# Optimization experiments

Measured on AMD Instinct MI355X. Metric: run time of the kernel, lower is better.

The kernel has to match this reference:

```python
import jax, jax.numpy as jnp
import numpy as np

BN, S, D = 200, 128, 1024          # B*N entity rows, scenes, d_model
D_INNER, D_STATE, D_CONV = 2048, 32, 4


def setup_inputs() -> dict:
    key = jax.random.key(0)
    ks = jax.random.split(key, 8)
    s = 0.02
    return {
        "x": jax.random.normal(ks[0], (BN, S, D), jnp.float32),
        "emotion_bias": jax.random.uniform(ks[1], (BN, S, 1), jnp.float32),
        "norm_w": jnp.ones((D,), jnp.float32),
        "norm_b": jnp.zeros((D,), jnp.float32),
        "in_proj_W": jax.random.normal(ks[2], (2 * D_INNER, D), jnp.float32) * s,
        "conv_w": jax.random.normal(ks[3], (D_INNER, 1, D_CONV), jnp.float32) * 0.1,
        "conv_b": jnp.zeros((D_INNER,), jnp.float32),
        "x_proj_W": jax.random.normal(ks[4], (2 * D_STATE + 1, D_INNER), jnp.float32) * s,
        "dt_W": jax.random.normal(ks[5], (D_INNER, 1), jnp.float32),
        "dt_b": jnp.zeros((D_INNER,), jnp.float32),
        "out_W": jax.random.normal(ks[6], (D, D_INNER), jnp.float32) * s,
        "emotion_scale": jnp.array(0.1, jnp.float32),
    }


def reference(x, emotion_bias, norm_w, norm_b, in_proj_W, conv_w, conv_b,
              x_proj_W, dt_W, dt_b, out_W, emotion_scale):
    residual = x
    # LayerNorm (eps=1e-5, biased variance as in torch)
    mu = x.mean(-1, keepdims=True)
    var = ((x - mu) ** 2).mean(-1, keepdims=True)
    xn = (x - mu) * jax.lax.rsqrt(var + 1e-5) * norm_w + norm_b

    xz = xn @ in_proj_W.T                      # [BN, S, 2*d_inner]
    x_in, z = jnp.split(xz, 2, axis=-1)

    # causal depthwise conv1d (torch pads d_conv-1 both sides, truncates to S == left-pad only)
    xc = jax.lax.conv_general_dilated(
        x_in.transpose(0, 2, 1), conv_w,
        window_strides=(1,), padding=[(D_CONV - 1, 0)],
        feature_group_count=D_INNER,
        dimension_numbers=("NCH", "OIH", "NCH"))
    xc = (xc + conv_b[None, :, None]).transpose(0, 2, 1)   # [BN, S, d_inner]
    x_act = jax.nn.silu(xc)

    x_ssm = x_act @ x_proj_W.T                 # [BN, S, 2*d_state+1]
    delta_raw, B_mat, C = jnp.split(x_ssm, [1, 1 + D_STATE], axis=-1)
    delta = jax.nn.softplus(delta_raw @ dt_W.T + dt_b)     # [BN, S, d_inner]
    delta = jnp.maximum(delta + emotion_scale * emotion_bias, 1e-4)

    def step(h, inp):
        d_t, B_t, C_t, xa_t = inp              # [BN,d_inner],[BN,n],[BN,n],[BN,d_inner]
        h = h * jnp.exp(-d_t)[..., None] + B_t[:, None, :] * xa_t[..., None]
        h = jnp.clip(h, -100.0, 100.0)
        y_t = jnp.einsum("bdn,bn->bd", h, C_t)
        return h, y_t

    h0 = jnp.zeros((BN, D_INNER, D_STATE), jnp.float32)
    xs = (delta.transpose(1, 0, 2), B_mat.transpose(1, 0, 2),
          C.transpose(1, 0, 2), x_act.transpose(1, 0, 2))
    _, y = jax.lax.scan(step, h0, xs)          # y: [S, BN, d_inner]
    y = y.transpose(1, 0, 2)

    return (y * jax.nn.silu(z)) @ out_W.T + residual
```

## Files before the change

kernel.cpp:

```cpp
#include <hip/hip_runtime.h>
#include <cstdint>
#include <cstddef>

#define NBN   200
#define NS    128
#define ND    1024
#define NDI   2048
#define NST   32
#define NROWS (NBN * NS)

typedef __attribute__((ext_vector_type(8))) short bf16x8;
typedef __attribute__((ext_vector_type(4))) float f32x4;

__device__ __forceinline__ unsigned short f2bf(float f) {
    unsigned int u = __float_as_uint(f);
    u += 0x7fffu + ((u >> 16) & 1u);
    return (unsigned short)(u >> 16);
}
__device__ __forceinline__ float bf2f(unsigned short h) {
    return __uint_as_float(((unsigned int)h) << 16);
}

__device__ __forceinline__ void gl_lds16(const void* g, void* l) {
    typedef __attribute__((address_space(1))) const unsigned int* gp_t;
    typedef __attribute__((address_space(3))) unsigned int* lp_t;
    __builtin_amdgcn_global_load_lds((gp_t)(uintptr_t)g,
                                     (lp_t)(unsigned int)(uintptr_t)l, 16, 0, 0);
}

__global__ __launch_bounds__(256) void cvt_kernel(const float* __restrict__ src,
                                                  unsigned short* __restrict__ dst, int n) {
    int i = blockIdx.x * 256 + threadIdx.x;
    if (i < n) dst[i] = f2bf(src[i]);
}

__global__ __launch_bounds__(256) void padwx_kernel(const float* __restrict__ src,
                                                    unsigned short* __restrict__ dst) {
    int i = blockIdx.x * 256 + threadIdx.x;
    int r = i >> 11;
    dst[i] = (r < 65) ? f2bf(src[i]) : (unsigned short)0;
}

__global__ __launch_bounds__(256) void ln_kernel(const float* __restrict__ x,
                                                 const float* __restrict__ gw,
                                                 const float* __restrict__ gb,
                                                 unsigned short* __restrict__ xn) {
    __shared__ float ss[4], ss2[4];
    size_t row = blockIdx.x;
    int tid = threadIdx.x;
    const float4* px = (const float4*)(x + row * ND);
    float4 v = px[tid];
    float s  = v.x + v.y + v.z + v.w;
    float s2 = fmaf(v.x, v.x, fmaf(v.y, v.y, fmaf(v.z, v.z, v.w * v.w)));
    #pragma unroll
    for (int off = 32; off > 0; off >>= 1) {
        s  += __shfl_down(s,  off, 64);
        s2 += __shfl_down(s2, off, 64);
    }
    if ((tid & 63) == 0) { ss[tid >> 6] = s; ss2[tid >> 6] = s2; }
    __syncthreads();
    float tot  = ss[0] + ss[1] + ss[2] + ss[3];
    float tot2 = ss2[0] + ss2[1] + ss2[2] + ss2[3];
    float mu   = tot * (1.f / ND);
    float var  = fmaf(tot2, 1.f / ND, -mu * mu);
    float rstd = rsqrtf(var + 1e-5f);
    float4 wv = ((const float4*)gw)[tid];
    float4 bv = ((const float4*)gb)[tid];
    ushort4 o;
    o.x = f2bf(fmaf((v.x - mu) * rstd, wv.x, bv.x));
    o.y = f2bf(fmaf((v.y - mu) * rstd, wv.y, bv.y));
    o.z = f2bf(fmaf((v.z - mu) * rstd, wv.z, bv.z));
    o.w = f2bf(fmaf((v.w - mu) * rstd, wv.w, bv.w));
    ((ushort4*)(xn + row * ND))[tid] = o;
}


#define BARRIER __builtin_amdgcn_s_barrier()
#define LGKM0  asm volatile("s_waitcnt lgkmcnt(0)" ::: "memory")
#define VMCNT6 asm volatile("s_waitcnt vmcnt(6)" ::: "memory")
#define VMCNT0 asm volatile("s_waitcnt vmcnt(0)" ::: "memory")
#define NOWAIT ((void)0)
#define PRIO1  __builtin_amdgcn_s_setprio(1)
#define PRIO0  __builtin_amdgcn_s_setprio(0)

#define STG_A(t, kp) {                                                        \
    gl_lds16(gA0 + (size_t)(t) * 64 + (kp) * 32,                              \
             lA + (((t) & 1) << 15) + ((kp) << 14));                          \
    gl_lds16(gA1 + (size_t)(t) * 64 + (kp) * 32,                              \
             lA + (((t) & 1) << 15) + ((kp) << 14) + 8192); }
#define STG_B(t, kp) {                                                        \
    gl_lds16(gB0 + (size_t)(t) * 64 + (kp) * 32,                              \
             lB + (((t) & 1) << 15) + ((kp) << 14));                          \
    gl_lds16(gB1 + (size_t)(t) * 64 + (kp) * 32,                              \
             lB + (((t) & 1) << 15) + ((kp) << 14) + 8192); }

#define RD_A(dst, mh, kp) { _Pragma("unroll")                                 \
    for (int mi = 0; mi < 4; ++mi)                                            \
        dst[mi] = *(const bf16x8*)(aRd + bo + (kp) * 16384 + (mh) * 4096 + mi * 1024); }
#define RD_B(dst, kp) { _Pragma("unroll")                                     \
    for (int ni = 0; ni < 4; ++ni)                                            \
        dst[ni] = *(const bf16x8*)(bRd + bo + (kp) * 16384 + ni * 1024); }

#define MM(mh, AV, BV) { _Pragma("unroll")                                    \
    for (int mi = 0; mi < 4; ++mi) { _Pragma("unroll")                        \
        for (int ni = 0; ni < 4; ++ni)                                        \
            acc[(mh) * 4 + mi][ni] = __builtin_amdgcn_mfma_f32_16x16x32_bf16( \
                AV[mi], BV[ni], acc[(mh) * 4 + mi][ni], 0, 0, 0); } }

#define TILE(t, DO_AP1, DO_T2, W) {                                           \
    const int bo = ((t) & 1) << 15;                                           \
                                                          \
    RD_A(aK0, 0, 0); RD_B(bK0, 0);                                            \
    if (DO_AP1) STG_A((t) + 1, 1);                                            \
    BARRIER; LGKM0; PRIO1; MM(0, aK0, bK0); PRIO0; BARRIER;                   \
                                                          \
    RD_A(aK1, 0, 1); RD_B(bK1, 1);                                            \
    if (DO_T2) STG_B((t) + 2, 0);                                             \
    BARRIER; LGKM0; PRIO1; MM(0, aK1, bK1); PRIO0; BARRIER;                   \
                                                          \
    RD_A(aK0, 1, 0);                                                          \
    if (DO_T2) STG_B((t) + 2, 1);                                             \
    BARRIER; LGKM0; PRIO1; MM(1, aK0, bK0); PRIO0; BARRIER;                   \
                                                          \
    RD_A(aK1, 1, 1);                                                          \
    if (DO_T2) STG_A((t) + 2, 0);                                             \
    BARRIER; LGKM0; PRIO1; MM(1, aK1, bK1); PRIO0;                            \
    W;                                                                        \
    BARRIER; }

template <int K, int EPI>
__global__ __launch_bounds__(512, 2)
void gemm256(const unsigned short* __restrict__ A,
             const unsigned short* __restrict__ B,
             int N, void* __restrict__ outp, const float* __restrict__ resid) {
    constexpr int NT = K / 64;
    static_assert(NT >= 3, "need >=3 K-tiles");
    __shared__ __align__(16) char smem[131072];

    const int tid  = threadIdx.x;
    const int lane = tid & 63;
    const int wid  = tid >> 6;
    const int lrow = lane & 15;
    const int kq   = lane >> 4;
    const int wmi  = wid >> 2;
    const int wni  = wid & 3;

    const int gx  = gridDim.x;
    const int nwg = gx * gridDim.y;
    const int lin = blockIdx.y * gx + blockIdx.x;
    const int id2 = (lin & 7) * (nwg >> 3) + (lin >> 3);
    const int bm  = id2 % gx;
    const int bn  = id2 / gx;

    const size_t m0 = (size_t)bm * 256;
    const size_t n0 = (size_t)bn * 256;

    const int fr = (lrow >> 1) & 3;
    const char* aRd = smem +          (wmi * 128 + lrow) * 64 + ((kq ^ fr) << 4);
    const char* bRd = smem + 65536 + (wni * 64  + lrow) * 64 + ((kq ^ fr) << 4);

    const int srow = wid * 16 + (lane >> 2);
    const int scol = (((lane & 3) ^ ((lane >> 3) & 3)) << 3);
    const unsigned short* gA0 = A + (m0 + srow) * K + scol;
    const unsigned short* gA1 = A + (m0 + 128 + srow) * K + scol;
    const unsigned short* gB0 = B + (n0 + srow) * K + scol;
    const unsigned short* gB1 = B + (n0 + 128 + srow) * K + scol;
    char* lA = smem + wid * 1024;
    char* lB = smem + 65536 + wid * 1024;

    f32x4 acc[8][4];
    #pragma unroll
    for (int i = 0; i < 8; ++i)
        #pragma unroll
        for (int j = 0; j < 4; ++j) acc[i][j] = (f32x4){0.f, 0.f, 0.f, 0.f};

    bf16x8 aK0[4], aK1[4], bK0[4], bK1[4];

    STG_B(0, 0); STG_B(0, 1); STG_A(0, 0); STG_A(0, 1);
    STG_B(1, 0); STG_B(1, 1); STG_A(1, 0);
    VMCNT6;
    BARRIER;

    int t = 0;
    #pragma unroll 2
    for (; t < NT - 2; ++t) { TILE(t, 1, 1, VMCNT6); }
    TILE((NT - 2), 1, 0, VMCNT0);
    TILE((NT - 1), 0, 0, NOWAIT);

    #pragma unroll
    for (int mi = 0; mi < 8; ++mi)
        #pragma unroll
        for (int ni = 0; ni < 4; ++ni)
            #pragma unroll
            for (int r = 0; r < 4; ++r) {
                size_t row = m0 + wmi * 128 + mi * 16 + kq * 4 + r;
                size_t col = n0 + wni * 64 + ni * 16 + lrow;
                size_t idx = row * (size_t)N + col;
                float v = acc[mi][ni][r];
                if (EPI == 0) ((unsigned short*)outp)[idx] = f2bf(v);
                else          ((float*)outp)[idx] = v + resid[idx];
            }
}

__global__ __launch_bounds__(256) void conv_silu_kernel(const unsigned short* __restrict__ xz,
                                                        const float* __restrict__ cw,
                                                        const float* __restrict__ cb,
                                                        unsigned short* __restrict__ xact) {
    int tid = blockIdx.x * 256 + threadIdx.x;
    int c = tid & (NDI - 1);
    int b = tid >> 11;
    float4 wv = ((const float4*)cw)[c];
    float w0 = wv.x, w1 = wv.y, w2 = wv.z, w3 = wv.w;
    float bias = cb[c];
    const unsigned short* px = xz + (size_t)b * NS * (2 * NDI) + c;
    unsigned short* po = xact + (size_t)b * NS * NDI + c;
    float x0 = 0.f, x1 = 0.f, x2 = 0.f;
    for (int t = 0; t < NS; t++) {
        float x3 = bf2f(px[(size_t)t * (2 * NDI)]);
        float v  = fmaf(x3, w3, fmaf(x2, w2, fmaf(x1, w1, fmaf(x0, w0, bias))));
        float s  = v * __builtin_amdgcn_rcpf(1.f + __expf(-v));
        po[(size_t)t * NDI] = f2bf(s);
        x0 = x1; x1 = x2; x2 = x3;
    }
}

__global__ __launch_bounds__(256, 2)
void gemm2_kernel(const unsigned short* __restrict__ A,
                  const unsigned short* __restrict__ B,
                  float* __restrict__ out) {
    __shared__ __align__(16) unsigned short As[64 * 32];
    __shared__ __align__(16) unsigned short Bs[80 * 32];
    const int tid  = threadIdx.x;
    const int bm   = blockIdx.x;
    const int wid  = tid >> 6;
    const int lane = tid & 63;
    const int lrow = lane & 15;
    const int kq   = lane >> 4;

    f32x4 acc[5];
    #pragma unroll
    for (int i = 0; i < 5; i++) acc[i] = (f32x4){0.f, 0.f, 0.f, 0.f};

    const int r1 = tid >> 2;
    const int c8 = (tid & 3) << 3;
    const unsigned short* gA1 = A + ((size_t)bm * 64 + r1) * NDI + c8;
    const unsigned short* gB1 = B + (size_t)r1 * NDI + c8;
    const unsigned short* gB2 = B + (size_t)(64 + r1) * NDI + c8;
    char* lA1 = (char*)As + wid * 1024;
    char* lB1 = (char*)Bs + wid * 1024;
    char* lB2 = (char*)Bs + 4096;

    for (int kt = 0; kt < NDI; kt += 32) {
        __syncthreads();
        gl_lds16(gA1, lA1);
        gl_lds16(gB1, lB1);
        if (tid < 64) gl_lds16(gB2, lB2);
        gA1 += 32; gB1 += 32; gB2 += 32;
        __syncthreads();
        bf16x8 af = *(const bf16x8*)&As[(wid * 16 + lrow) * 32 + kq * 8];
        #pragma unroll
        for (int ni = 0; ni < 5; ni++) {
            bf16x8 bfr = *(const bf16x8*)&Bs[(ni * 16 + lrow) * 32 + kq * 8];
            acc[ni] = __builtin_amdgcn_mfma_f32_16x16x32_bf16(af, bfr, acc[ni], 0, 0, 0);
        }
    }
    #pragma unroll
    for (int ni = 0; ni < 5; ni++)
        #pragma unroll
        for (int r = 0; r < 4; r++) {
            size_t row = (size_t)bm * 64 + wid * 16 + kq * 4 + r;
            int col = ni * 16 + lrow;
            out[row * 80 + col] = acc[ni][r];
        }
}

__global__ __launch_bounds__(256)
void scan_kernel(const float* __restrict__ xssm,
                 unsigned short* xact_g,
                 const unsigned short* __restrict__ xz,
                 const float* __restrict__ dtW,
                 const float* __restrict__ dtb,
                 const float* __restrict__ eb,
                 const float* __restrict__ es_p) {
    __shared__ __align__(16) float sB[NS][NST];
    __shared__ __align__(16) float sC[NS][NST];
    __shared__ float sDR[NS];
    __shared__ float sDE[NS];
    const int tid = threadIdx.x;
    const int b   = blockIdx.y;
    const int d   = blockIdx.x * 256 + tid;

    for (int i = tid; i < NS * 65; i += 256) {
        int t = i / 65, c = i - t * 65;
        float v = xssm[((size_t)b * NS + t) * 80 + c];
        if (c == 0)      sDR[t] = v;
        else if (c < 33) sB[t][c - 1] = v;
        else             sC[t][c - 33] = v;
    }
    {
        float es = es_p[0];
        for (int i = tid; i < NS; i += 256) sDE[i] = es * eb[b * NS + i];
    }
    __syncthreads();

    const float w  = dtW[d];
    const float bb = dtb[d];
    float h[NST];
    #pragma unroll
    for (int n = 0; n < NST; n++) h[n] = 0.f;

    unsigned short* p        = xact_g + (size_t)b * NS * NDI + d;
    const unsigned short* pz = xz + (size_t)b * NS * (2 * NDI) + NDI + d;

    for (int t = 0; t < NS; t++) {
        float xa = bf2f(*p);
        float zz = bf2f(*pz);
        float raw = fmaf(sDR[t], w, bb);
        float sp  = (raw > 20.f) ? raw : __logf(1.f + __expf(raw));
        float delta = fmaxf(sp + sDE[t], 1e-4f);
        float a = __expf(-delta);
        float y = 0.f;
        #pragma unroll
        for (int n8 = 0; n8 < 8; n8++) {
            f32x4 Bv = *(const f32x4*)&sB[t][n8 * 4];
            f32x4 Cv = *(const f32x4*)&sC[t][n8 * 4];
            #pragma unroll
            for (int j = 0; j < 4; j++) {
                h[n8 * 4 + j] = fmaf(h[n8 * 4 + j], a, Bv[j] * xa);
                y = fmaf(h[n8 * 4 + j], Cv[j], y);
            }
        }
        float sig = __builtin_amdgcn_rcpf(1.f + __expf(-zz));
        *p = f2bf(y * zz * sig);
        p += NDI; pz += 2 * NDI;
    }
}

extern "C" void kernel_launch(void* const* d_in, const int* in_sizes, int n_in,
                              void* d_out, int out_size, void* d_ws, size_t ws_size,
                              hipStream_t stream) {
    const float* x   = (const float*)d_in[0];
    const float* eb  = (const float*)d_in[1];
    const float* nw  = (const float*)d_in[2];
    const float* nb  = (const float*)d_in[3];
    const float* Wi  = (const float*)d_in[4];
    const float* cw  = (const float*)d_in[5];
    const float* cb  = (const float*)d_in[6];
    const float* Wx  = (const float*)d_in[7];
    const float* dtW = (const float*)d_in[8];
    const float* dtb = (const float*)d_in[9];
    const float* Wo  = (const float*)d_in[10];
    const float* es  = (const float*)d_in[11];
    float* out = (float*)d_out;

    char* ws = (char*)d_ws;
    unsigned short* wi_b   = (unsigned short*)(ws + 0);
    unsigned short* wo_b   = (unsigned short*)(ws + 8388608);
    unsigned short* wx_b   = (unsigned short*)(ws + 12582912);
    unsigned short* xz_b   = (unsigned short*)(ws + 12910592);
    unsigned short* xact_b = (unsigned short*)(ws + 222625792);
    float*          xssm   = (float*)(ws + 327483392);
    if (ws_size < (size_t)335675392) return;

    cvt_kernel<<<(2 * NDI * ND + 255) / 256, 256, 0, stream>>>(Wi, wi_b, 2 * NDI * ND);
    cvt_kernel<<<(ND * NDI + 255) / 256, 256, 0, stream>>>(Wo, wo_b, ND * NDI);
    padwx_kernel<<<(80 * NDI) / 256, 256, 0, stream>>>(Wx, wx_b);

    unsigned short* xn_b = xact_b;
    ln_kernel<<<NROWS, 256, 0, stream>>>(x, nw, nb, xn_b);

    gemm256<ND, 0><<<dim3(NROWS / 256, (2 * NDI) / 256), 512, 0, stream>>>(
        xn_b, wi_b, 2 * NDI, xz_b, nullptr);

    conv_silu_kernel<<<(NBN * NDI) / 256, 256, 0, stream>>>(xz_b, cw, cb, xact_b);

    gemm2_kernel<<<NROWS / 64, 256, 0, stream>>>(xact_b, wx_b, xssm);

    scan_kernel<<<dim3(NDI / 256, NBN), 256, 0, stream>>>(xssm, xact_b, xz_b, dtW, dtb, eb, es);

    gemm256<NDI, 1><<<dim3(NROWS / 256, ND / 256), 512, 0, stream>>>(
        xact_b, wo_b, ND, out, x);
}
```

Baseline: 960.7 us.

## Replace sequential selective scan with chunked SSD matrix formulation on MFMA

Replaces the per-timestep recurrent scan with a chunked state-space-dual formulation. Each chunk of 32 timesteps builds a masked C·Bᵀ matrix and cumulative-decay-scaled inputs, then computes intra-chunk outputs and inter-chunk state carry with bf16 MFMA instead of 32-wide scalar FMAs per step. It aims to turn the latency-bound serial recurrence into matrix-core work with only four sequential chunk steps. The cost is more shared memory and barriers, a bf16 hidden state, and exp(+L) scaling inside a chunk, which can lose precision or overflow when decays are large.

New measurement: 882.4 us. 1.09x faster.

```diff
diff --git a/kernel.cpp b/kernel.cpp
--- a/kernel.cpp
+++ b/kernel.cpp
@@ -109,19 +109,15 @@
 
 #define TILE(t, DO_AP1, DO_T2, W) {                                           \
     const int bo = ((t) & 1) << 15;                                           \
-                                                          \
     RD_A(aK0, 0, 0); RD_B(bK0, 0);                                            \
     if (DO_AP1) STG_A((t) + 1, 1);                                            \
     BARRIER; LGKM0; PRIO1; MM(0, aK0, bK0); PRIO0; BARRIER;                   \
-                                                          \
     RD_A(aK1, 0, 1); RD_B(bK1, 1);                                            \
     if (DO_T2) STG_B((t) + 2, 0);                                             \
     BARRIER; LGKM0; PRIO1; MM(0, aK1, bK1); PRIO0; BARRIER;                   \
-                                                          \
     RD_A(aK0, 1, 0);                                                          \
     if (DO_T2) STG_B((t) + 2, 1);                                             \
     BARRIER; LGKM0; PRIO1; MM(1, aK0, bK0); PRIO0; BARRIER;                   \
-                                                          \
     RD_A(aK1, 1, 1);                                                          \
     if (DO_T2) STG_A((t) + 2, 0);                                             \
     BARRIER; LGKM0; PRIO1; MM(1, aK1, bK1); PRIO0;                            \
@@ -274,65 +270,156 @@
         }
 }
 
-__global__ __launch_bounds__(256)
-void scan_kernel(const float* __restrict__ xssm,
-                 unsigned short* xact_g,
-                 const unsigned short* __restrict__ xz,
-                 const float* __restrict__ dtW,
-                 const float* __restrict__ dtb,
-                 const float* __restrict__ eb,
-                 const float* __restrict__ es_p) {
-    __shared__ __align__(16) float sB[NS][NST];
-    __shared__ __align__(16) float sC[NS][NST];
-    __shared__ float sDR[NS];
-    __shared__ float sDE[NS];
-    const int tid = threadIdx.x;
-    const int b   = blockIdx.y;
-    const int d   = blockIdx.x * 256 + tid;
-
-    for (int i = tid; i < NS * 65; i += 256) {
-        int t = i / 65, c = i - t * 65;
-        float v = xssm[((size_t)b * NS + t) * 80 + c];
-        if (c == 0)      sDR[t] = v;
-        else if (c < 33) sB[t][c - 1] = v;
-        else             sC[t][c - 33] = v;
-    }
-    {
-        float es = es_p[0];
-        for (int i = tid; i < NS; i += 256) sDE[i] = es * eb[b * NS + i];
-    }
-    __syncthreads();
-
-    const float w  = dtW[d];
-    const float bb = dtb[d];
-    float h[NST];
-    #pragma unroll
-    for (int n = 0; n < NST; n++) h[n] = 0.f;
-
-    unsigned short* p        = xact_g + (size_t)b * NS * NDI + d;
-    const unsigned short* pz = xz + (size_t)b * NS * (2 * NDI) + NDI + d;
-
-    for (int t = 0; t < NS; t++) {
-        float xa = bf2f(*p);
-        float zz = bf2f(*pz);
-        float raw = fmaf(sDR[t], w, bb);
-        float sp  = (raw > 20.f) ? raw : __logf(1.f + __expf(raw));
-        float delta = fmaxf(sp + sDE[t], 1e-4f);
-        float a = __expf(-delta);
-        float y = 0.f;
-        #pragma unroll
-        for (int n8 = 0; n8 < 8; n8++) {
-            f32x4 Bv = *(const f32x4*)&sB[t][n8 * 4];
-            f32x4 Cv = *(const f32x4*)&sC[t][n8 * 4];
+__global__ __launch_bounds__(256, 2)
+void ssd_kernel(const float* __restrict__ xssm,
+                unsigned short* xact_g,
+                const unsigned short* __restrict__ xz,
+                const float* __restrict__ dtW,
+                const float* __restrict__ dtb,
+                const float* __restrict__ eb,
+                const float* __restrict__ es_p) {
+    __shared__ float sDR[32], sDE[32];
+    __shared__ __align__(16) unsigned short sC[32][32];
+    __shared__ __align__(16) unsigned short sB[32][32];
+    __shared__ __align__(16) unsigned short sBt[32][32];
+    __shared__ __align__(16) unsigned short sG[32][32];
+    __shared__ __align__(16) unsigned short sP[256][32];
+    __shared__ __align__(16) float          sE[256][32];
+    __shared__ __align__(16) unsigned short sH[256][32];
+
+    const int tid  = threadIdx.x;
+    const int b    = blockIdx.y;
+    const int d0   = blockIdx.x * 256;
+    const int lane = tid & 63;
+    const int wid  = tid >> 6;
+    const int lrow = lane & 15;
+    const int kq   = lane >> 4;
+    const int wd0  = wid * 64;
+
+    const float w  = dtW[d0 + tid];
+    const float bb = dtb[d0 + tid];
+    const float es = es_p[0];
+
+    for (int i = tid; i < 256 * 32; i += 256) ((unsigned short*)sH)[i] = 0;
+
+    #pragma unroll 1
+    for (int c = 0; c < 4; ++c) {
+        __syncthreads();
+        {
+            const float* src = xssm + ((size_t)b * 128 + c * 32) * 80;
+            for (int i = tid; i < 2560; i += 256) {
+                int t = i / 80, col = i - t * 80;
+                float v = src[i];
+                if (col == 0) sDR[t] = v;
+                else if (col < 33) {
+                    unsigned short bv = f2bf(v);
+                    sB[t][col - 1] = bv;
+                    sBt[col - 1][t] = bv;
+                } else if (col < 65) sC[t][col - 33] = f2bf(v);
+            }
+            if (tid < 32) sDE[tid] = es * eb[b * 128 + c * 32 + tid];
+        }
+        __syncthreads();
+
+        {
+            int mi = wid >> 1, ni = wid & 1;
+            bf16x8 af = *(const bf16x8*)&sC[mi * 16 + lrow][kq * 8];
+            bf16x8 bf = *(const bf16x8*)&sB[ni * 16 + lrow][kq * 8];
+            f32x4 z4 = (f32x4){0.f, 0.f, 0.f, 0.f};
+            f32x4 g = __builtin_amdgcn_mfma_f32_16x16x32_bf16(af, bf, z4, 0, 0, 0);
             #pragma unroll
-            for (int j = 0; j < 4; j++) {
-                h[n8 * 4 + j] = fmaf(h[n8 * 4 + j], a, Bv[j] * xa);
-                y = fmaf(h[n8 * 4 + j], Cv[j], y);
-            }
-        }
-        float sig = __builtin_amdgcn_rcpf(1.f + __expf(-zz));
-        *p = f2bf(y * zz * sig);
-        p += NDI; pz += 2 * NDI;
+            for (int r = 0; r < 4; ++r) {
+                int t = mi * 16 + kq * 4 + r, s = ni * 16 + lrow;
+                float val = (s <= t) ? g[r] : 0.f;
+                *(unsigned short*)((char*)sG + t * 64 +
+                    ((((s >> 3) ^ (t & 3)) << 4) | ((s & 7) << 1))) = f2bf(val);
+            }
+        }
+
+        {
+            const unsigned short* pxa =
+                xact_g + ((size_t)b * 128 + c * 32) * 2048 + d0 + tid;
+            float L = 0.f;
+            for (int t8 = 0; t8 < 4; ++t8) {
+                bf16x8 pv;
+                #pragma unroll
+                for (int j = 0; j < 8; ++j) {
+                    int t = t8 * 8 + j;
+                    float raw = fmaf(sDR[t], w, bb);
+                    float sp  = (raw > 20.f) ? raw : __logf(1.f + __expf(raw));
+                    float delta = fmaxf(sp + sDE[t], 1e-4f);
+                    L += delta;
+                    float xa = bf2f(pxa[(size_t)t * 2048]);
+                    pv[j] = (short)f2bf(xa * __expf(L));
+                    *(float*)((char*)sE + tid * 128 +
+                        ((((t >> 2) ^ (tid & 7)) << 4) | ((t & 3) << 2))) = __expf(-L);
+                }
+                *(bf16x8*)((char*)sP + tid * 64 + (((t8 ^ (tid & 3)) << 4))) = pv;
+            }
+        }
+        __syncthreads();
+
+        f32x4 acc[2][4], racc[2][4];
+        bf16x8 cfrag[2], gfrag[2], btfrag[2], hfrag[4], pfrag[4];
+        #pragma unroll
+        for (int mi = 0; mi < 2; ++mi) {
+            int tr = mi * 16 + lrow;
+            cfrag[mi]  = *(const bf16x8*)&sC[tr][kq * 8];
+            gfrag[mi]  = *(const bf16x8*)((const char*)sG + tr * 64 +
+                                          (((kq ^ (tr & 3)) << 4)));
+            btfrag[mi] = *(const bf16x8*)&sBt[tr][kq * 8];
+        }
+        #pragma unroll
+        for (int ni = 0; ni < 4; ++ni) {
+            int dc = wd0 + ni * 16 + lrow;
+            hfrag[ni] = *(const bf16x8*)&sH[dc][kq * 8];
+            pfrag[ni] = *(const bf16x8*)((const char*)sP + dc * 64 +
+                                         (((kq ^ (dc & 3)) << 4)));
+        }
+        #pragma unroll
+        for (int mi = 0; mi < 2; ++mi)
+            #pragma unroll
+            for (int ni = 0; ni < 4; ++ni) {
+                f32x4 z4 = (f32x4){0.f, 0.f, 0.f, 0.f};
+                acc[mi][ni] = __builtin_amdgcn_mfma_f32_16x16x32_bf16(
+                    cfrag[mi], hfrag[ni], z4, 0, 0, 0);
+                acc[mi][ni] = __builtin_amdgcn_mfma_f32_16x16x32_bf16(
+                    gfrag[mi], pfrag[ni], acc[mi][ni], 0, 0, 0);
+                racc[mi][ni] = __builtin_amdgcn_mfma_f32_16x16x32_bf16(
+                    btfrag[mi], pfrag[ni], z4, 0, 0, 0);
+            }
+
+        #pragma unroll
+        for (int mi = 0; mi < 2; ++mi)
+            #pragma unroll
+            for (int ni = 0; ni < 4; ++ni) {
+                int dc = wd0 + ni * 16 + lrow;
+                f32x4 ev = *(const f32x4*)((const char*)sE + dc * 128 +
+                                           ((((mi * 4 + kq) ^ (dc & 7)) << 4)));
+                size_t rowg = (size_t)b * 128 + c * 32 + mi * 16 + kq * 4;
+                #pragma unroll
+                for (int r = 0; r < 4; ++r) {
+                    float y  = acc[mi][ni][r] * ev[r];
+                    float zz = bf2f(xz[(rowg + r) * 4096 + 2048 + d0 + dc]);
+                    float sig = __builtin_amdgcn_rcpf(1.f + __expf(-zz));
+                    xact_g[(rowg + r) * 2048 + d0 + dc] = f2bf(y * zz * sig);
+                }
+            }
+
+        #pragma unroll
+        for (int ni = 0; ni < 4; ++ni) {
+            int dc = wd0 + ni * 16 + lrow;
+            float e31 = *(const float*)((const char*)sE + dc * 128 +
+                                        (((7 ^ (dc & 7)) << 4) | 12));
+            #pragma unroll
+            for (int mi = 0; mi < 2; ++mi)
+                #pragma unroll
+                for (int r = 0; r < 4; ++r) {
+                    int n = mi * 16 + kq * 4 + r;
+                    float h = bf2f(sH[dc][n]) + racc[mi][ni][r];
+                    sH[dc][n] = f2bf(e31 * h);
+                }
+        }
     }
 }
 
@@ -376,7 +463,7 @@
 
     gemm2_kernel<<<NROWS / 64, 256, 0, stream>>>(xact_b, wx_b, xssm);
 
-    scan_kernel<<<dim3(NDI / 256, NBN), 256, 0, stream>>>(xssm, xact_b, xz_b, dtW, dtb, eb, es);
+    ssd_kernel<<<dim3(NDI / 256, NBN), 256, 0, stream>>>(xssm, xact_b, xz_b, dtW, dtb, eb, es);
 
     gemm256<NDI, 1><<<dim3(NROWS / 256, ND / 256), 512, 0, stream>>>(
         xact_b, wo_b, ND, out, x);
```
